# Kernel tuning notes

Measured on AMD Instinct MI355X. Metric: run time of the kernel, lower is better.

Reference implementation:

```python
import math
import jax, jax.numpy as jnp
import numpy as np

EMBED_DIM = 768
NUM_HEADS = 12
HEAD_DIM = EMBED_DIM // NUM_HEADS


def setup_inputs() -> dict:
    key = jax.random.key(0)
    ks = jax.random.split(key, 9)
    R, C, B, E = 128, 512, 1, EMBED_DIM
    x = jax.random.normal(ks[0], (R, C, B, E), dtype=jnp.float32)
    s = 0.02
    # weights stored so that projection is x @ W + b (i.e. torch Linear weight transposed)
    Wq = jax.random.normal(ks[1], (E, E), dtype=jnp.float32) * s
    Wk = jax.random.normal(ks[2], (E, E), dtype=jnp.float32) * s
    Wv = jax.random.normal(ks[3], (E, E), dtype=jnp.float32) * s
    Wo = jax.random.normal(ks[4], (E, E), dtype=jnp.float32) * s
    bq = jnp.zeros((E,), jnp.float32)
    bk = jnp.zeros((E,), jnp.float32)
    bv = jnp.zeros((E,), jnp.float32)
    bo = jnp.zeros((E,), jnp.float32)
    return {"x": x, "Wq": Wq, "bq": bq, "Wk": Wk, "bk": bk,
            "Wv": Wv, "bv": bv, "Wo": Wo, "bo": bo}


def reference(x, Wq, bq, Wk, bk, Wv, bv, Wo, bo):
    R, C, B, E = x.shape
    H, D = NUM_HEADS, HEAD_DIM
    # scaling = head_dim^-0.5 / sqrt(num_rows)  (align_scaling)
    scaling = (D ** -0.5) / math.sqrt(R)
    q = (x @ Wq + bq).reshape(R, C, B, H, D) * scaling
    k = (x @ Wk + bk).reshape(R, C, B, H, D)
    v = (x @ Wv + bv).reshape(R, C, B, H, D)
    # sum attention logits over rows r -> shared [h, n, i, j] attention map
    attn_weights = jnp.einsum('rinhd,rjnhd->hnij', q, k)
    attn_probs = jax.nn.softmax(attn_weights, axis=-1)
    context = jnp.einsum('hnij,rjnhd->rinhd', attn_probs, v)
    context = context.reshape(R, C, B, E)
    output = context @ Wo + bo
    return output, attn_probs
```

## Files before the change

kernel.cpp:

```cpp
#include <hip/hip_runtime.h>
#include <math.h>

#define RDIM 128
#define CDIM 512
#define EDIM 768
#define HDIM 12
#define DDIM 64
#define MDIM (RDIM*CDIM)
#define OUT_ELEMS ((size_t)MDIM*EDIM)
#define HSTRIDE ((size_t)CDIM*RDIM*DDIM)
#define WELEMS (EDIM*EDIM)

typedef unsigned short ushort_t;
typedef __attribute__((ext_vector_type(8))) short bf16x8;
typedef __attribute__((ext_vector_type(8))) unsigned short u16x8;
typedef __attribute__((ext_vector_type(4))) float f32x4;

__device__ __forceinline__ ushort_t f2bf(float f) {
    unsigned u = __float_as_uint(f);
    unsigned r = u + 0x7fffu + ((u >> 16) & 1u);
    return (ushort_t)(r >> 16);
}

__device__ __forceinline__ void gload16(const void* g, void* l) {
    __builtin_amdgcn_global_load_lds(
        (const __attribute__((address_space(1))) unsigned int*)g,
        (__attribute__((address_space(3))) unsigned int*)l, 16, 0, 0);
}

__global__ __launch_bounds__(256)
void cast_x(const float* __restrict__ x, ushort_t* __restrict__ xb) {
    size_t i = ((size_t)blockIdx.x * 256 + threadIdx.x) * 8;
    float4 a = *(const float4*)&x[i];
    float4 b = *(const float4*)&x[i + 4];
    u16x8 o;
    o[0]=f2bf(a.x); o[1]=f2bf(a.y); o[2]=f2bf(a.z); o[3]=f2bf(a.w);
    o[4]=f2bf(b.x); o[5]=f2bf(b.y); o[6]=f2bf(b.z); o[7]=f2bf(b.w);
    *(u16x8*)&xb[i] = o;
}

__global__ __launch_bounds__(256)
void transpose_cast_w(const float* __restrict__ W, ushort_t* __restrict__ Wt) {
    __shared__ ushort_t t[64][66];
    const int k0 = blockIdx.x * 64, n0 = blockIdx.y * 64;
    const int tx = threadIdx.x & 15, ty = threadIdx.x >> 4;
    #pragma unroll
    for (int rep = 0; rep < 4; ++rep) {
        int k = ty + rep * 16;
        float4 v = *(const float4*)&W[(size_t)(k0 + k) * EDIM + n0 + tx*4];
        t[k][tx*4+0] = f2bf(v.x); t[k][tx*4+1] = f2bf(v.y);
        t[k][tx*4+2] = f2bf(v.z); t[k][tx*4+3] = f2bf(v.w);
    }
    __syncthreads();
    #pragma unroll
    for (int rep = 0; rep < 4; ++rep) {
        int n = ty + rep * 16;
        ushort4 o = { t[tx*4+0][n], t[tx*4+1][n], t[tx*4+2][n], t[tx*4+3][n] };
        *(ushort4*)&Wt[(size_t)(n0 + n) * EDIM + k0 + tx*4] = o;
    }
}

__global__ __launch_bounds__(256)
void concat_bias(const float* __restrict__ bq, const float* __restrict__ bk,
                 const float* __restrict__ bv, float* __restrict__ bqkv) {
    int i = blockIdx.x * 256 + threadIdx.x;
    if (i < 768)        bqkv[i] = bq[i];
    else if (i < 1536)  bqkv[i] = bk[i - 768];
    else if (i < 2304)  bqkv[i] = bv[i - 1536];
}

#define SBAR do { __builtin_amdgcn_sched_barrier(0); \
                  __builtin_amdgcn_s_barrier(); \
                  __builtin_amdgcn_sched_barrier(0); } while(0)
#define SCHED0 __builtin_amdgcn_sched_barrier(0)
#define VMCNT(n_) asm volatile("s_waitcnt vmcnt(" #n_ ")" ::: "memory")

template<int M, int N, int K, int LDK, int MODE, int NWG>
__global__ __launch_bounds__(512, 2)
void gemm8(const ushort_t* __restrict__ A, const ushort_t* __restrict__ B,
           const float* __restrict__ bias, float scale,
           float* __restrict__ outF, ushort_t* __restrict__ outB,
           size_t sAh, size_t sBh) {
    __shared__ __align__(16) char smem[131072];
    constexpr int NT = K / 64;

    const int tid = threadIdx.x;
    const int lane = tid & 63, wid = tid >> 6;
    const int wr = wid >> 2, wc = wid & 3;
    const int fr = lane & 15, fs = lane >> 4;
    const int sw = (fr & 7) << 3;

    const int bid = blockIdx.x;
    const int w = (bid & 7) * (NWG / 8) + (bid >> 3);
    int bm, bn, h = 0, ksub = 0, plane = 0, ntile = 0;
    if (MODE == 4)      { ntile = w % 9; bm = (w / 9) * 256; bn = ntile * 256; }
    else if (MODE == 2) { plane = w >> 2; h = plane >> 3; ksub = plane & 7;
                          bm = ((w >> 1) & 1) * 256; bn = (w & 1) * 256; }
    else if (MODE == 3) { h = w >> 6; bm = ((w >> 5) & 1) * 256; bn = (w & 31) * 256; }
    else                { bm = (w / 3) * 256; bn = (w % 3) * 256; }

    const ushort_t* Ab = A + (MODE == 2 || MODE == 3 ? (size_t)h * sAh : 0)
                       + (MODE == 2 ? (size_t)ksub * K : 0) + (size_t)bm * LDK;
    const ushort_t* Bb = B + (MODE == 2 || MODE == 3 ? (size_t)h * sBh : 0)
                       + (MODE == 2 ? (size_t)ksub * K : 0) + (size_t)bn * LDK;

    const int r0 = tid >> 3, s0 = tid & 7;
    const size_t gO0 = (size_t)r0 * LDK + ((s0 ^ (r0 & 7)) * 8);
    const size_t gO1 = gO0 + (size_t)64 * LDK;
    const int l0 = tid * 16, l1 = tid * 16 + 8192;

#define STAGE_A(t_, h_) do { \
    char* d_ = smem + ((((t_) & 1) * 2 + (h_)) * 16384); \
    const ushort_t* s_ = Ab + (size_t)((h_) * 128) * LDK + (t_) * 64; \
    gload16(s_ + gO0, d_ + l0); gload16(s_ + gO1, d_ + l1); } while(0)
#define STAGE_B(t_, h_) do { \
    char* d_ = smem + 65536 + ((((t_) & 1) * 2 + (h_)) * 16384); \
    const ushort_t* s_ = Bb + (size_t)((h_) * 128) * LDK + (t_) * 64; \
    gload16(s_ + gO0, d_ + l0); gload16(s_ + gO1, d_ + l1); } while(0)

    f32x4 acc[8][4];
    #pragma unroll
    for (int i = 0; i < 8; ++i)
        #pragma unroll
        for (int j = 0; j < 4; ++j) acc[i][j] = (f32x4){0.f, 0.f, 0.f, 0.f};
    bf16x8 a_[4][2], a2_[4][2], bb0_[2][2], bb1_[2][2];

#define DSA(t_, mq_, A_) do { \
    const ushort_t* As_ = (const ushort_t*)(smem + ((((t_) & 1) * 2 + wr) * 16384)); \
    _Pragma("unroll") for (int f = 0; f < 4; ++f) \
      _Pragma("unroll") for (int kk = 0; kk < 2; ++kk) \
        A_[f][kk] = *(const bf16x8*)&As_[((mq_) * 64 + f * 16 + fr) * 64 \
                                          + ((kk * 32 + fs * 8) ^ sw)]; } while(0)

#define DSB(t_, nq_, B_) do { \
    const ushort_t* Bs_ = (const ushort_t*)(smem + 65536 + ((((t_) & 1) * 2 + (wc >> 1)) * 16384)); \
    _Pragma("unroll") for (int nf = 0; nf < 2; ++nf) \
      _Pragma("unroll") for (int kk = 0; kk < 2; ++kk) \
        B_[nf][kk] = *(const bf16x8*)&Bs_[((wc & 1) * 64 + (nq_) * 32 + nf * 16 + fr) * 64 \
                                           + ((kk * 32 + fs * 8) ^ sw)]; } while(0)

#define MFMA8(mq_, nq_, A_, B_) do { \
    __builtin_amdgcn_s_setprio(1); \
    _Pragma("unroll") for (int f = 0; f < 4; ++f) \
      _Pragma("unroll") for (int nf2 = 0; nf2 < 2; ++nf2) \
        _Pragma("unroll") for (int kk = 0; kk < 2; ++kk) \
          acc[(mq_) * 4 + f][(nq_) * 2 + nf2] = __builtin_amdgcn_mfma_f32_16x16x32_bf16( \
              A_[f][kk], B_[nf2][kk], acc[(mq_) * 4 + f][(nq_) * 2 + nf2], 0, 0, 0); \
    __builtin_amdgcn_s_setprio(0); } while(0)

    STAGE_B(0, 0); SCHED0;
    STAGE_B(0, 1); SCHED0;
    STAGE_A(0, 0); SCHED0;
    STAGE_A(0, 1); SCHED0;
    STAGE_B(1, 0); SCHED0;
    STAGE_B(1, 1); SCHED0;
    STAGE_A(1, 0); SCHED0;
    STAGE_A(1, 1); SCHED0;
    VMCNT(8);
    SBAR;
    DSA(0, 0, a_); DSB(0, 0, bb0_);

    for (int t = 0; t < NT - 2; ++t) {
        DSB(t, 1, bb1_);
        MFMA8(0, 0, a_, bb0_);
        SBAR;
        DSA(t, 1, a2_);
        MFMA8(0, 1, a_, bb1_);
        VMCNT(0);
        SBAR;
        DSA(t + 1, 0, a_);
        STAGE_B(t + 2, 0); STAGE_B(t + 2, 1);
        MFMA8(1, 0, a2_, bb0_);
        SBAR;
        DSB(t + 1, 0, bb0_);
        STAGE_A(t + 2, 0); STAGE_A(t + 2, 1);
        MFMA8(1, 1, a2_, bb1_);
        SBAR;
    }

    {
        const int t = NT - 2;
        DSB(t, 1, bb1_);      MFMA8(0, 0, a_, bb0_);  SBAR;
        DSA(t, 1, a2_);       MFMA8(0, 1, a_, bb1_);
        VMCNT(0);             SBAR;
        DSA(t + 1, 0, a_);    MFMA8(1, 0, a2_, bb0_); SBAR;
        DSB(t + 1, 0, bb0_);  MFMA8(1, 1, a2_, bb1_); SBAR;
        const int u = NT - 1;
        DSB(u, 1, bb1_);      MFMA8(0, 0, a_, bb0_);  SBAR;
        DSA(u, 1, a2_);       MFMA8(0, 1, a_, bb1_);  SBAR;
        MFMA8(1, 0, a2_, bb0_);
        MFMA8(1, 1, a2_, bb1_);
    }

    if (MODE == 4) {
        const int which = ntile / 3;
        const int hcb = (ntile % 3) * 256;
        if (which < 2) {
            ushort_t* dst = outB + (size_t)which * OUT_ELEMS;
            const float sc = (which == 0) ? scale : 1.f;
            #pragma unroll
            for (int mf = 0; mf < 8; ++mf) {
                #pragma unroll
                for (int nf = 0; nf < 4; ++nf) {
                    const int hcol = hcb + wc*64 + nf*16 + fr;
                    const float bv = bias[which*768 + hcol];
                    const int hh = hcol >> 6, d = hcol & 63;
                    #pragma unroll
                    for (int j = 0; j < 4; ++j) {
                        const int m = bm + wr*128 + mf*16 + fs*4 + j;
                        float v = (acc[mf][nf][j] + bv) * sc;
                        size_t addr = (size_t)hh * HSTRIDE
                                    + (size_t)(m & 511) * 8192 + (m >> 9) * 64 + d;
                        dst[addr] = f2bf(v);
                    }
                }
            }
        } else {
            ushort_t* Ts = (ushort_t*)smem;
            ushort_t* dst = outB + 2 * OUT_ELEMS;
            const int rblk = bm >> 9, jb = bm & 511;
            __syncthreads();
            #pragma unroll
            for (int q = 0; q < 2; ++q) {
                if ((wc >> 1) == q) {
                    #pragma unroll
                    for (int mf = 0; mf < 8; ++mf) {
                        #pragma unroll
                        for (int nf = 0; nf < 4; ++nf) {
                            const int nl = wc*64 + nf*16 + fr;
                            const float bv = bias[1536 + hcb + nl];
                            #pragma unroll
                            for (int j = 0; j < 4; ++j)
                                Ts[(nl & 127)*264 + wr*128 + mf*16 + fs*4 + j] =
                                    f2bf(acc[mf][nf][j] + bv);
                        }
                    }
                }
                __syncthreads();
                #pragma unroll
                for (int it = 0; it < 8; ++it) {
                    const int idx = it * 512 + tid;
                    const int row = idx >> 5, c8 = (idx & 31) * 8;
                    const int nl = q*128 + row;
                    const int hh = (hcb + nl) >> 6, d = nl & 63;
                    uint4 wv;
                    wv.x = *(const uint*)&Ts[row*264 + c8];
                    wv.y = *(const uint*)&Ts[row*264 + c8 + 2];
                    wv.z = *(const uint*)&Ts[row*264 + c8 + 4];
                    wv.w = *(const uint*)&Ts[row*264 + c8 + 6];
                    size_t addr = (size_t)hh * HSTRIDE
                                + (size_t)(rblk*64 + d) * CDIM + jb + c8;
                    *(uint4*)&dst[addr] = wv;
                }
                __syncthreads();
            }
        }
        return;
    }

    #pragma unroll
    for (int mf = 0; mf < 8; ++mf) {
        #pragma unroll
        for (int nf = 0; nf < 4; ++nf) {
            const int n = bn + wc*64 + nf*16 + fr;
            float bv = (MODE == 1) ? bias[n] : 0.f;
            #pragma unroll
            for (int j = 0; j < 4; ++j) {
                const int m = bm + wr*128 + mf*16 + fs*4 + j;
                float v = acc[mf][nf][j];
                if (MODE == 1) {
                    outF[(size_t)m * N + n] = v + bv;
                } else if (MODE == 2) {
                    outF[(size_t)plane * (CDIM*CDIM) + (size_t)m * CDIM + n] = v;
                } else {
                    size_t addr = ((size_t)(n >> 6) * CDIM + m) * EDIM
                                + h * DDIM + (n & 63);
                    outB[addr] = f2bf(v);
                }
            }
        }
    }
}

__global__ __launch_bounds__(256)
void softmax_reduce(const float* __restrict__ part, float* __restrict__ attn,
                    ushort_t* __restrict__ Pb) {
    const int row = blockIdx.x;
    const int h = row >> 9, c = row & 511;
    const int tid = threadIdx.x;
    const int lane = tid & 63, wid = tid >> 6;
    __shared__ float red[8];

    float v0 = 0.f, v1 = 0.f;
    #pragma unroll
    for (int s = 0; s < 8; ++s) {
        const float* p = part + ((size_t)(h*8 + s) * (CDIM*CDIM)) + (size_t)c * CDIM;
        v0 += p[tid];
        v1 += p[tid + 256];
    }
    float m = fmaxf(v0, v1);
    #pragma unroll
    for (int off = 32; off > 0; off >>= 1) m = fmaxf(m, __shfl_down(m, off));
    if (lane == 0) red[wid] = m;
    __syncthreads();
    if (tid == 0) red[4] = fmaxf(fmaxf(red[0], red[1]), fmaxf(red[2], red[3]));
    __syncthreads();
    const float M = red[4];

    float e0 = expf(v0 - M), e1 = expf(v1 - M);
    float s = e0 + e1;
    #pragma unroll
    for (int off = 32; off > 0; off >>= 1) s += __shfl_down(s, off);
    __syncthreads();
    if (lane == 0) red[wid] = s;
    __syncthreads();
    if (tid == 0) red[5] = red[0] + red[1] + red[2] + red[3];
    __syncthreads();
    const float inv = 1.f / red[5];
    float o0 = e0 * inv, o1 = e1 * inv;
    float* pout = attn + (size_t)row * CDIM;
    ushort_t* pb = Pb + (size_t)row * CDIM;
    pout[tid] = o0;        pout[tid + 256] = o1;
    pb[tid]   = f2bf(o0);  pb[tid + 256]   = f2bf(o1);
}

extern "C" void kernel_launch(void* const* d_in, const int* in_sizes, int n_in,
                              void* d_out, int out_size, void* d_ws, size_t ws_size,
                              hipStream_t stream) {
    const float* x  = (const float*)d_in[0];
    const float* Wq = (const float*)d_in[1];
    const float* bq = (const float*)d_in[2];
    const float* Wk = (const float*)d_in[3];
    const float* bk = (const float*)d_in[4];
    const float* Wv = (const float*)d_in[5];
    const float* bv = (const float*)d_in[6];
    const float* Wo = (const float*)d_in[7];
    const float* bo = (const float*)d_in[8];

    float* out   = (float*)d_out;
    float* attnp = out + OUT_ELEMS;

    ushort_t* ws   = (ushort_t*)d_ws;
    ushort_t* xb   = ws;
    ushort_t* Wqkv = xb + OUT_ELEMS;
    ushort_t* Wto  = Wqkv + 3*WELEMS;
    float*    bqkv = (float*)(Wto + WELEMS);
    ushort_t* Qp   = Wto + WELEMS + 4608;
    ushort_t* Kp   = Qp + OUT_ELEMS;
    ushort_t* Vt   = Kp + OUT_ELEMS;
    ushort_t* Pb   = Vt + OUT_ELEMS;
    float*    part = (float*)xb;
    ushort_t* ctxb = xb;

    const float scaling = 0.011048543456039806f;

    cast_x<<<MDIM*EDIM/(256*8), 256, 0, stream>>>(x, xb);
    dim3 wt(EDIM/64, EDIM/64);
    transpose_cast_w<<<wt, 256, 0, stream>>>(Wq, Wqkv);
    transpose_cast_w<<<wt, 256, 0, stream>>>(Wk, Wqkv + WELEMS);
    transpose_cast_w<<<wt, 256, 0, stream>>>(Wv, Wqkv + 2*WELEMS);
    transpose_cast_w<<<wt, 256, 0, stream>>>(Wo, Wto);
    concat_bias<<<9, 256, 0, stream>>>(bq, bk, bv, bqkv);

    gemm8<MDIM, 2304, EDIM, EDIM, 4, 2304><<<2304, 512, 0, stream>>>(
        xb, Wqkv, bqkv, scaling, nullptr, Qp, 0, 0);

    gemm8<CDIM, CDIM, 1024, 8192, 2, 384><<<384, 512, 0, stream>>>(
        Qp, Kp, nullptr, 1.f, part, nullptr, HSTRIDE, HSTRIDE);

    softmax_reduce<<<HDIM*CDIM, 256, 0, stream>>>(part, attnp, Pb);

    gemm8<CDIM, 8192, CDIM, CDIM, 3, 768><<<768, 512, 0, stream>>>(
        Pb, Vt, nullptr, 1.f, nullptr, ctxb, (size_t)CDIM*CDIM, HSTRIDE);

    gemm8<MDIM, EDIM, EDIM, EDIM, 1, 768><<<768, 512, 0, stream>>>(
        ctxb, Wto, bo, 1.f, out, nullptr, 0, 0);
}
```

Measured before the change: 598.0 us.

## Restructure GEMM main loop into finer-grained load/compute phases with explicit LDS waits

Reorganizes the gemm8 pipeline so each of the four MFMA quadrant phases is preceded by its own LDS reads and one global-to-LDS stage issue, instead of batching two stage issues per phase. The prologue stages A only for tile 0, and A for tile t+1 is now issued inside iteration t. Explicit lgkmcnt(0) waits plus extra barriers are added before each MFMA group. The aim is to spread global loads evenly and overlap them with compute, at the cost of more barriers and waits per iteration.

```diff
diff --git a/kernel.cpp b/kernel.cpp
--- a/kernel.cpp
+++ b/kernel.cpp
@@ -72,7 +72,8 @@
 #define SBAR do { __builtin_amdgcn_sched_barrier(0); \
                   __builtin_amdgcn_s_barrier(); \
                   __builtin_amdgcn_sched_barrier(0); } while(0)
-#define SCHED0 __builtin_amdgcn_sched_barrier(0)
+#define LGKM0 do { asm volatile("s_waitcnt lgkmcnt(0)" ::: "memory"); \
+                   __builtin_amdgcn_sched_barrier(0); } while(0)
 #define VMCNT(n_) asm volatile("s_waitcnt vmcnt(" #n_ ")" ::: "memory")
 
 template<int M, int N, int K, int LDK, int MODE, int NWG>
@@ -148,47 +149,59 @@
               A_[f][kk], B_[nf2][kk], acc[(mq_) * 4 + f][(nq_) * 2 + nf2], 0, 0, 0); \
     __builtin_amdgcn_s_setprio(0); } while(0)
 
-    STAGE_B(0, 0); SCHED0;
-    STAGE_B(0, 1); SCHED0;
-    STAGE_A(0, 0); SCHED0;
-    STAGE_A(0, 1); SCHED0;
-    STAGE_B(1, 0); SCHED0;
-    STAGE_B(1, 1); SCHED0;
-    STAGE_A(1, 0); SCHED0;
-    STAGE_A(1, 1); SCHED0;
-    VMCNT(8);
+    STAGE_B(0, 0); __builtin_amdgcn_sched_barrier(0);
+    STAGE_B(0, 1); __builtin_amdgcn_sched_barrier(0);
+    STAGE_A(0, 0); __builtin_amdgcn_sched_barrier(0);
+    STAGE_A(0, 1); __builtin_amdgcn_sched_barrier(0);
+    STAGE_B(1, 0); __builtin_amdgcn_sched_barrier(0);
+    STAGE_B(1, 1); __builtin_amdgcn_sched_barrier(0);
+    VMCNT(4);
     SBAR;
-    DSA(0, 0, a_); DSB(0, 0, bb0_);
 
     for (int t = 0; t < NT - 2; ++t) {
-        DSB(t, 1, bb1_);
+        DSA(t, 0, a_); DSB(t, 0, bb0_);
+        STAGE_A(t + 1, 0);
+        SBAR; LGKM0;
         MFMA8(0, 0, a_, bb0_);
         SBAR;
+        DSB(t, 1, bb1_);
+        STAGE_A(t + 1, 1);
+        SBAR; LGKM0;
+        MFMA8(0, 1, a_, bb1_);
+        SBAR;
         DSA(t, 1, a2_);
-        MFMA8(0, 1, a_, bb1_);
-        VMCNT(0);
-        SBAR;
-        DSA(t + 1, 0, a_);
-        STAGE_B(t + 2, 0); STAGE_B(t + 2, 1);
+        STAGE_B(t + 2, 0);
+        SBAR; LGKM0;
         MFMA8(1, 0, a2_, bb0_);
         SBAR;
-        DSB(t + 1, 0, bb0_);
-        STAGE_A(t + 2, 0); STAGE_A(t + 2, 1);
+        STAGE_B(t + 2, 1);
+        VMCNT(4);
+        SBAR; LGKM0;
         MFMA8(1, 1, a2_, bb1_);
         SBAR;
     }
 
     {
         const int t = NT - 2;
-        DSB(t, 1, bb1_);      MFMA8(0, 0, a_, bb0_);  SBAR;
-        DSA(t, 1, a2_);       MFMA8(0, 1, a_, bb1_);
-        VMCNT(0);             SBAR;
-        DSA(t + 1, 0, a_);    MFMA8(1, 0, a2_, bb0_); SBAR;
-        DSB(t + 1, 0, bb0_);  MFMA8(1, 1, a2_, bb1_); SBAR;
+        DSA(t, 0, a_); DSB(t, 0, bb0_);
+        STAGE_A(t + 1, 0);
+        SBAR; LGKM0; MFMA8(0, 0, a_, bb0_); SBAR;
+        DSB(t, 1, bb1_);
+        STAGE_A(t + 1, 1);
+        SBAR; LGKM0; MFMA8(0, 1, a_, bb1_); SBAR;
+        DSA(t, 1, a2_);
+        SBAR; LGKM0; MFMA8(1, 0, a2_, bb0_); SBAR;
+        VMCNT(0);
+        SBAR; LGKM0; MFMA8(1, 1, a2_, bb1_); SBAR;
+    }
+    {
         const int u = NT - 1;
-        DSB(u, 1, bb1_);      MFMA8(0, 0, a_, bb0_);  SBAR;
-        DSA(u, 1, a2_);       MFMA8(0, 1, a_, bb1_);  SBAR;
-        MFMA8(1, 0, a2_, bb0_);
+        DSA(u, 0, a_); DSB(u, 0, bb0_);
+        SBAR; LGKM0; MFMA8(0, 0, a_, bb0_); SBAR;
+        DSB(u, 1, bb1_);
+        SBAR; LGKM0; MFMA8(0, 1, a_, bb1_); SBAR;
+        DSA(u, 1, a2_);
+        SBAR; LGKM0; MFMA8(1, 0, a2_, bb0_); SBAR;
         MFMA8(1, 1, a2_, bb1_);
     }
 
```

Result: no change. 601.0 us (+0.5%).
